# Performance work log

Hardware: AMD Instinct MI355X
Metric: run time of the kernel (lower is better)

Reference implementation:

```python
import jax, jax.numpy as jnp
import numpy as np

V, D, H, O = 32000, 256, 512, 6
B, T = 128, 2048


def setup_inputs() -> dict:
    key = jax.random.key(0)
    ks = jax.random.split(key, 8)
    s = lambda k, shp, fan: jax.random.normal(k, shp, jnp.float32) / np.float32(np.sqrt(fan))
    return dict(
        token_ids=jax.random.randint(ks[0], (B, T), 0, V),
        emb=s(ks[1], (V, D), D),
        gru_wih=s(ks[2], (3 * H, D), D),
        gru_whh=s(ks[3], (3 * H, H), H),
        gru_b=jnp.zeros((3 * H,), jnp.float32),
        gru_bn=jnp.zeros((H,), jnp.float32),
        lstm_wih=s(ks[4], (4 * H, H), H),
        lstm_whh=s(ks[5], (4 * H, H), H),
        lstm_b=jnp.zeros((4 * H,), jnp.float32),
        head_w=s(ks[6], (O, H), H),
        head_b=jnp.zeros((O,), jnp.float32),
    )


def reference(token_ids, emb, gru_wih, gru_whh, gru_b, gru_bn,
              lstm_wih, lstm_whh, lstm_b, head_w, head_b):
    x = emb[token_ids]                      # (B, T, D) embedding lookup
    xs = jnp.swapaxes(x, 0, 1)              # (T, B, D) for scan over time
    h = gru_whh.shape[1]
    h0 = jnp.zeros((x.shape[0], h), x.dtype)

    def step(carry, xt):
        hg, hl, cl = carry
        # --- equinox GRUCell ---
        ig = xt @ gru_wih.T + gru_b         # (B, 3H)
        hh = hg @ gru_whh.T                 # (B, 3H)
        ir, iz, inn = jnp.split(ig, 3, axis=-1)
        hr, hz, hn = jnp.split(hh, 3, axis=-1)
        r = jax.nn.sigmoid(ir + hr)
        z = jax.nn.sigmoid(iz + hz)
        n = jnp.tanh(inn + r * (hn + gru_bn))
        hg_new = n + z * (hg - n)           # == (1-z)*n + z*hg
        # --- equinox LSTMCell (input = GRU output) ---
        lin = hg_new @ lstm_wih.T + hl @ lstm_whh.T + lstm_b  # (B, 4H)
        i_, f_, g_, o_ = jnp.split(lin, 4, axis=-1)
        c_new = jax.nn.sigmoid(f_) * cl + jax.nn.sigmoid(i_) * jnp.tanh(g_)
        h_new = jax.nn.sigmoid(o_) * jnp.tanh(c_new)
        return (hg_new, h_new, c_new), None

    (_, h_final, _), _ = jax.lax.scan(step, (h0, h0, h0), xs)
    return h_final @ head_w.T + head_b      # (B, O)
```

## Files before the change

### kernel.cpp

```cpp
#include <hip/hip_runtime.h>
#include <hip/hip_bf16.h>


typedef short v8s __attribute__((ext_vector_type(8)));
typedef float v4f __attribute__((ext_vector_type(4)));
typedef unsigned long long u64;

#define T_STEPS 2048
#define RING_OFF 8192
#define DYN_LDS 150816

#define MFMA16(a, b, c) __builtin_amdgcn_mfma_f32_16x16x32_bf16((a), (b), (c), 0, 0, 0)

__device__ __forceinline__ v4f v4zero() { v4f z = {0.f, 0.f, 0.f, 0.f}; return z; }
__device__ __forceinline__ float sigf(float x) { return 1.f / (1.f + __expf(-x)); }
__device__ __forceinline__ float tanhf_fast(float x) { return 1.f - 2.f / (1.f + __expf(2.f * x)); }

__device__ __forceinline__ ushort f2us(float v) {
  __hip_bfloat16 b = __float2bfloat16(v);
  return *reinterpret_cast<ushort*>(&b);
}
__device__ __forceinline__ float us2f(ushort u) {
  __hip_bfloat16 b;
  *reinterpret_cast<ushort*>(&b) = u;
  return __bfloat162float(b);
}
__device__ __forceinline__ void cvt_hilo(float v, ushort& h, ushort& l) {
  __hip_bfloat16 bh = __float2bfloat16(v);
  float r = v - __bfloat162float(bh);
  __hip_bfloat16 bl = __float2bfloat16(r);
  h = *reinterpret_cast<ushort*>(&bh);
  l = *reinterpret_cast<ushort*>(&bl);
}
__device__ __forceinline__ void stage4(ushort* hi, ushort* lo, const float* src) {
  float4 v = *(const float4*)src;
  float a[4] = {v.x, v.y, v.z, v.w};
#pragma unroll
  for (int j = 0; j < 4; ++j) { ushort h, l; cvt_hilo(a[j], h, l); hi[j] = h; lo[j] = l; }
}
__device__ __forceinline__ void stage4h(ushort* hi, const float* src) {
  float4 v = *(const float4*)src;
  float a[4] = {v.x, v.y, v.z, v.w};
#pragma unroll
  for (int j = 0; j < 4; ++j) hi[j] = f2us(a[j]);
}
__device__ __forceinline__ void st_wt(ushort* p, ushort v) {
  __hip_atomic_store(p, v, __ATOMIC_RELAXED, __HIP_MEMORY_SCOPE_AGENT);
}
__device__ __forceinline__ void st_row32(ushort* rowp, int r16, ushort uh) {
  unsigned v32 = (unsigned)uh;
  unsigned nb = (unsigned)__shfl_xor((int)v32, 1);
  if (!(r16 & 1)) v32 |= (nb << 16);
  unsigned hi32 = (unsigned)__shfl_xor((int)v32, 2);
  if ((r16 & 3) == 0) {
    u64 v = (u64)v32 | ((u64)hi32 << 32);
    __hip_atomic_store((u64*)(rowp + r16), v, __ATOMIC_RELAXED, __HIP_MEMORY_SCOPE_AGENT);
  }
}
__device__ __forceinline__ v8s ld_a16(const ushort* p) {
  u64 a = __hip_atomic_load((const u64*)p, __ATOMIC_RELAXED, __HIP_MEMORY_SCOPE_AGENT);
  u64 b = __hip_atomic_load((const u64*)p + 1, __ATOMIC_RELAXED, __HIP_MEMORY_SCOPE_AGENT);
  union { u64 u[2]; v8s v; } r;
  r.u[0] = a; r.u[1] = b;
  return r.v;
}

__device__ __forceinline__ int poll_ge(const int* p, int tgt, long& budget) {
  while (budget > 0) {
    if (__hip_atomic_load(p, __ATOMIC_RELAXED, __HIP_MEMORY_SCOPE_AGENT) >= tgt) return 1;
    __builtin_amdgcn_s_sleep(1);
    --budget;
  }
  return 0;
}
__device__ __forceinline__ int pollep(const int* gepo, int ta,
                                      const int* lepo, int tb,
                                      int lane, long& budget, int& slack) {
  const int* p = (lane < 32) ? (gepo + lane) : (lepo + (lane - 32));
  const int t = (lane < 32) ? ta : tb;
  while (budget > 0) {
    int v = __hip_atomic_load(p, __ATOMIC_RELAXED, __HIP_MEMORY_SCOPE_AGENT);
    int d = v - t;
    if (__all(d >= 0)) {
      int m = d;
#pragma unroll
      for (int off = 1; off < 64; off <<= 1) {
        int o = __shfl_xor(m, off);
        m = (o < m) ? o : m;
      }
      slack = m;
      return 1;
    }
    __builtin_amdgcn_s_sleep(1);
    --budget;
  }
  return 0;
}

__global__ void __launch_bounds__(256, 1) rnn_persistent(
    const int* __restrict__ tok,
    const float* __restrict__ emb,
    const float* __restrict__ gwih,
    const float* __restrict__ gwhh,
    const float* __restrict__ gb,
    const float* __restrict__ gbn,
    const float* __restrict__ lwih,
    const float* __restrict__ lwhh,
    const float* __restrict__ lb,
    char* __restrict__ ws,
    int hstride, int has_lo)
{
  extern __shared__ char smem[];
  const int tid  = threadIdx.x;
  const int wgid = blockIdx.x;
  const bool is_gru = (wgid < 64);
  const int sub = is_gru ? wgid : (wgid - 64);
  const int bg  = sub & 1;
  const int cg  = sub >> 1;
  const int colbase = cg * 16;
  const int b0 = bg * 64;
  const int lane = tid & 63;
  const int wave = tid >> 6;
  const int quad = lane >> 4;
  const int r16  = lane & 15;

  int* cnt = (int*)ws;
  int* gru_ep  = cnt + bg * 32;
  int* lstm_ep = cnt + 64 + bg * 32;
  int* boot    = cnt + 128;
  ushort* ring = (ushort*)(ws + RING_OFF);
  const int slotE = 128 * hstride;
  ushort* hlb = ring + 2 * slotE;

  const int mrow  = wave * 16 + r16;
  const int bglob = b0 + wave * 16 + quad * 4;
  const int col   = colbase + r16;
  long budget = 3000000;
  int slack = 0;

  if (is_gru) {
    ushort* smemU = (ushort*)smem;
    const int WIH_HI = 0, WIH_LO = 12672, WHH_HI = 25344, WHH_LO = 50304;
    int* okf = (int*)(smem + 150528);

    for (int i = tid; i < 48 * 64; i += 256) {
      int row = i >> 6, q = (i & 63) * 4;
      int gate = row >> 4, c = colbase + (row & 15);
      stage4(&smemU[WIH_HI + row * 264 + q], &smemU[WIH_LO + row * 264 + q],
             gwih + (long)(gate * 512 + c) * 256 + q);
    }
    for (int i = tid; i < 48 * 128; i += 256) {
      int row = i >> 7, k = (i & 127) * 4;
      int gate = row >> 4, c = colbase + (row & 15);
      stage4(&smemU[WHH_HI + row * 520 + k], &smemU[WHH_LO + row * 520 + k],
             gwhh + (long)(gate * 512 + c) * 512 + k);
    }
    const float b_r  = gb[col];
    const float b_z  = gb[512 + col];
    const float b_in = gb[1024 + col];
    const float bnv  = gbn[col];
    __syncthreads();

    if (tid == 0) {
      __hip_atomic_fetch_add(boot, 1, __ATOMIC_RELEASE, __HIP_MEMORY_SCOPE_AGENT);
      long bb = 3000000;
      okf[0] = poll_ge(boot, 128, bb);
    }
    __syncthreads();
    if (!okf[0]) { if (wgid == 0 && tid == 0) st_wt(&hlb[slotE + 0], f2us(1.0e4f)); return; }

    v4f acc_r, acc_z, acc_nx;
    float hgreg[4] = {0.f, 0.f, 0.f, 0.f};
    float4 xa[16];

    auto prefetch_x = [&](int tn) {
      int ntok = tok[(b0 + mrow) * T_STEPS + tn];
      const float* xrow = emb + (long)ntok * 256;
#pragma unroll
      for (int kk = 0; kk < 8; ++kk) {
        xa[2 * kk]     = *(const float4*)(xrow + kk * 32 + quad * 8);
        xa[2 * kk + 1] = *(const float4*)(xrow + kk * 32 + quad * 8 + 4);
      }
    };
    auto accx_compute = [&]() {
      acc_r = v4zero(); acc_z = v4zero(); acc_nx = v4zero();
#pragma unroll
      for (int kk = 0; kk < 8; ++kk) {
        float xv[8] = {xa[2 * kk].x, xa[2 * kk].y, xa[2 * kk].z, xa[2 * kk].w,
                       xa[2 * kk + 1].x, xa[2 * kk + 1].y, xa[2 * kk + 1].z, xa[2 * kk + 1].w};
        v8s ahi, alo;
#pragma unroll
        for (int j = 0; j < 8; ++j) { ushort h, l; cvt_hilo(xv[j], h, l); ahi[j] = (short)h; alo[j] = (short)l; }
        const int orr = (r16) * 264 + kk * 32 + quad * 8;
        const int oz  = (16 + r16) * 264 + kk * 32 + quad * 8;
        const int on  = (32 + r16) * 264 + kk * 32 + quad * 8;
        v8s brh = *(const v8s*)&smemU[WIH_HI + orr], brl = *(const v8s*)&smemU[WIH_LO + orr];
        v8s bzh = *(const v8s*)&smemU[WIH_HI + oz],  bzl = *(const v8s*)&smemU[WIH_LO + oz];
        v8s bnh = *(const v8s*)&smemU[WIH_HI + on],  bnl = *(const v8s*)&smemU[WIH_LO + on];
        acc_r = MFMA16(ahi, brh, acc_r); acc_r = MFMA16(alo, brh, acc_r); acc_r = MFMA16(ahi, brl, acc_r);
        acc_z = MFMA16(ahi, bzh, acc_z); acc_z = MFMA16(alo, bzh, acc_z); acc_z = MFMA16(ahi, bzl, acc_z);
        acc_nx = MFMA16(ahi, bnh, acc_nx); acc_nx = MFMA16(alo, bnh, acc_nx); acc_nx = MFMA16(ahi, bnl, acc_nx);
      }
    };

    prefetch_x(0);
    accx_compute();

    for (int t = 0; t < T_STEPS; ++t) {
      if (t + 1 < T_STEPS) prefetch_x(t + 1);

      if (t > 0) {
        if (wave == 0) {
          int ok = 1;
          if (slack > 0) { --slack; }
          else ok = pollep(gru_ep, t, lstm_ep, t - 1, lane, budget, slack);
          if (lane == 0) okf[0] = ok;
        }
        __syncthreads();
        if (!okf[0]) { if (tid == 0) st_wt(&hlb[slotE + 2 + wgid], f2us(100.f)); break; }
      }

      v8s ahi[16], alo[16];
      if (t > 0) {
        const ushort* hrow = ring + ((t - 1) & 1) * slotE + (b0 + mrow) * hstride;
#pragma unroll
        for (int kk = 0; kk < 16; ++kk) {
          ahi[kk] = ld_a16(&hrow[kk * 32 + quad * 8]);
          if (has_lo) alo[kk] = ld_a16(&hrow[512 + kk * 32 + quad * 8]);
        }
      }

      v4f acc_nh = v4zero();
      if (t > 0) {
#pragma unroll
        for (int kk = 0; kk < 16; ++kk) {
          const int orr = (r16) * 520 + kk * 32 + quad * 8;
          const int oz  = (16 + r16) * 520 + kk * 32 + quad * 8;
          const int on  = (32 + r16) * 520 + kk * 32 + quad * 8;
          v8s brh = *(const v8s*)&smemU[WHH_HI + orr], brl = *(const v8s*)&smemU[WHH_LO + orr];
          v8s bzh = *(const v8s*)&smemU[WHH_HI + oz],  bzl = *(const v8s*)&smemU[WHH_LO + oz];
          v8s bnh = *(const v8s*)&smemU[WHH_HI + on],  bnl = *(const v8s*)&smemU[WHH_LO + on];
          acc_r = MFMA16(ahi[kk], brh, acc_r); acc_r = MFMA16(ahi[kk], brl, acc_r);
          acc_z = MFMA16(ahi[kk], bzh, acc_z); acc_z = MFMA16(ahi[kk], bzl, acc_z);
          acc_nh = MFMA16(ahi[kk], bnh, acc_nh); acc_nh = MFMA16(ahi[kk], bnl, acc_nh);
          if (has_lo) {
            acc_r = MFMA16(alo[kk], brh, acc_r);
            acc_z = MFMA16(alo[kk], bzh, acc_z);
            acc_nh = MFMA16(alo[kk], bnh, acc_nh);
          }
        }
      }

      ushort* slotT = ring + (t & 1) * slotE;
#pragma unroll
      for (int rg = 0; rg < 4; ++rg) {
        float r = sigf(acc_r[rg] + b_r);
        float z = sigf(acc_z[rg] + b_z);
        float nn = tanhf_fast(acc_nx[rg] + b_in + r * (acc_nh[rg] + bnv));
        float hnew = nn + z * (hgreg[rg] - nn);
        hgreg[rg] = hnew;
        ushort uh = f2us(hnew);
        ushort* rp = &slotT[(bglob + rg) * hstride + colbase];
        st_row32(rp, r16, uh);
        if (has_lo) st_row32(rp + 512, r16, f2us(hnew - us2f(uh)));
      }

      __syncthreads();
      if (tid == 0)
        __hip_atomic_store(gru_ep + cg, t + 1, __ATOMIC_RELEASE, __HIP_MEMORY_SCOPE_AGENT);
      if (t + 1 < T_STEPS) accx_compute();
    }
  } else {
    ushort* smemU = (ushort*)smem;
    int* okf = (int*)(smem + 132096);

    for (int i = tid; i < 64 * 256; i += 256) {
      int row = i >> 8, k = (i & 255) * 4;
      int gate = row >> 4, c = colbase + (row & 15);
      long grow = gate * 512 + c;
      const float* src = (k < 512) ? (lwih + grow * 512 + k) : (lwhh + grow * 512 + (k - 512));
      stage4h(&smemU[row * 1032 + k], src);
    }
    const float b_i = lb[col];
    const float b_f = lb[512 + col];
    const float b_g = lb[1024 + col];
    const float b_o = lb[1536 + col];
    __syncthreads();

    if (tid == 0) {
      __hip_atomic_fetch_add(boot, 1, __ATOMIC_RELEASE, __HIP_MEMORY_SCOPE_AGENT);
      long bb = 3000000;
      okf[0] = poll_ge(boot, 128, bb);
    }
    __syncthreads();
    if (!okf[0]) { if (wgid == 64 && tid == 0) st_wt(&hlb[slotE + 1], f2us(1.0e4f)); return; }

    float creg[4] = {0.f, 0.f, 0.f, 0.f};

    for (int t = 0; t < T_STEPS; ++t) {
      if (wave == 0) {
        int ok = 1;
        if (slack > 0) { --slack; }
        else ok = pollep(gru_ep, t + 1, lstm_ep, t, lane, budget, slack);
        if (lane == 0) okf[0] = ok;
      }
      __syncthreads();
      if (!okf[0]) { if (tid == 0) st_wt(&hlb[slotE + 2 + wgid], f2us(100.f)); break; }

      v8s ghi[16], glo[16];
      {
        const ushort* hrow = ring + (t & 1) * slotE + (b0 + mrow) * hstride;
#pragma unroll
        for (int kk = 0; kk < 16; ++kk) {
          ghi[kk] = ld_a16(&hrow[kk * 32 + quad * 8]);
          if (has_lo) glo[kk] = ld_a16(&hrow[512 + kk * 32 + quad * 8]);
        }
      }
      v8s lhi[16], llo[16];
      const ushort* lrow = hlb + ((t - 1) & 1) * slotE + (b0 + mrow) * hstride;
      if (t > 0) {
#pragma unroll
        for (int kk = 0; kk < 16; ++kk) lhi[kk] = ld_a16(&lrow[kk * 32 + quad * 8]);
      }

      v4f ai = v4zero(), af = v4zero(), ag = v4zero(), ao = v4zero();
#pragma unroll
      for (int kk = 0; kk < 16; ++kk) {
        v8s bi = *(const v8s*)&smemU[(r16) * 1032 + kk * 32 + quad * 8];
        v8s bf = *(const v8s*)&smemU[(16 + r16) * 1032 + kk * 32 + quad * 8];
        v8s bgv = *(const v8s*)&smemU[(32 + r16) * 1032 + kk * 32 + quad * 8];
        v8s bo = *(const v8s*)&smemU[(48 + r16) * 1032 + kk * 32 + quad * 8];
        ai = MFMA16(ghi[kk], bi, ai); af = MFMA16(ghi[kk], bf, af);
        ag = MFMA16(ghi[kk], bgv, ag); ao = MFMA16(ghi[kk], bo, ao);
        if (has_lo) {
          ai = MFMA16(glo[kk], bi, ai); af = MFMA16(glo[kk], bf, af);
          ag = MFMA16(glo[kk], bgv, ag); ao = MFMA16(glo[kk], bo, ao);
        }
      }

      if (t > 0) {
        if (has_lo) {
#pragma unroll
          for (int kk = 0; kk < 16; ++kk) llo[kk] = ld_a16(&lrow[512 + kk * 32 + quad * 8]);
        }
#pragma unroll
        for (int kk = 0; kk < 16; ++kk) {
          v8s bi = *(const v8s*)&smemU[(r16) * 1032 + 512 + kk * 32 + quad * 8];
          v8s bf = *(const v8s*)&smemU[(16 + r16) * 1032 + 512 + kk * 32 + quad * 8];
          v8s bgv = *(const v8s*)&smemU[(32 + r16) * 1032 + 512 + kk * 32 + quad * 8];
          v8s bo = *(const v8s*)&smemU[(48 + r16) * 1032 + 512 + kk * 32 + quad * 8];
          ai = MFMA16(lhi[kk], bi, ai); af = MFMA16(lhi[kk], bf, af);
          ag = MFMA16(lhi[kk], bgv, ag); ao = MFMA16(lhi[kk], bo, ao);
        }
        if (has_lo) {
#pragma unroll
          for (int kk = 0; kk < 16; ++kk) {
            v8s bi = *(const v8s*)&smemU[(r16) * 1032 + 512 + kk * 32 + quad * 8];
            v8s bf = *(const v8s*)&smemU[(16 + r16) * 1032 + 512 + kk * 32 + quad * 8];
            v8s bgv = *(const v8s*)&smemU[(32 + r16) * 1032 + 512 + kk * 32 + quad * 8];
            v8s bo = *(const v8s*)&smemU[(48 + r16) * 1032 + 512 + kk * 32 + quad * 8];
            ai = MFMA16(llo[kk], bi, ai); af = MFMA16(llo[kk], bf, af);
            ag = MFMA16(llo[kk], bgv, ag); ao = MFMA16(llo[kk], bo, ao);
          }
        }
      }

      ushort* hout = hlb + (t & 1) * slotE;
#pragma unroll
      for (int rg = 0; rg < 4; ++rg) {
        float i_ = sigf(ai[rg] + b_i), f_ = sigf(af[rg] + b_f);
        float g_ = tanhf_fast(ag[rg] + b_g), o_ = sigf(ao[rg] + b_o);
        float cn = f_ * creg[rg] + i_ * g_;
        creg[rg] = cn;
        float hv = o_ * tanhf_fast(cn);
        ushort uh = f2us(hv);
        ushort* rp = &hout[(bglob + rg) * hstride + colbase];
        st_row32(rp, r16, uh);
        if (has_lo) st_row32(rp + 512, r16, f2us(hv - us2f(uh)));
      }

      __syncthreads();
      if (tid == 0)
        __hip_atomic_store(lstm_ep + cg, t + 1, __ATOMIC_RELEASE, __HIP_MEMORY_SCOPE_AGENT);
    }
  }
}

__global__ void head_kernel(const char* __restrict__ ws,
                            const float* __restrict__ hw,
                            const float* __restrict__ hbias,
                            float* __restrict__ out,
                            int hstride, int has_lo) {
  const ushort* h1 = (const ushort*)(ws + RING_OFF) + 3 * 128 * hstride;
  const int b = blockIdx.x, l = threadIdx.x;
  const int k0 = l * 8;
  v8s hi = ld_a16(&h1[b * hstride + k0]);
  v8s lo;
  if (has_lo) lo = ld_a16(&h1[b * hstride + 512 + k0]);
  float acc[6] = {0.f, 0.f, 0.f, 0.f, 0.f, 0.f};
#pragma unroll
  for (int j = 0; j < 8; ++j) {
    float h = us2f((ushort)hi[j]);
    if (has_lo) h += us2f((ushort)lo[j]);
#pragma unroll
    for (int o = 0; o < 6; ++o) acc[o] += h * hw[o * 512 + k0 + j];
  }
#pragma unroll
  for (int o = 0; o < 6; ++o) {
    float v = acc[o];
    for (int off = 32; off > 0; off >>= 1) v += __shfl_down(v, off);
    if (l == 0) out[b * 6 + o] = v + hbias[o];
  }
}

__global__ void init_ws(int* cnt) {
  int i = blockIdx.x * blockDim.x + threadIdx.x;
  if (i < 2048)
    __hip_atomic_store(cnt + i, 0, __ATOMIC_RELAXED, __HIP_MEMORY_SCOPE_AGENT);
}

__global__ void ws_too_small_marker(float* out) {
  if (threadIdx.x == 0 && blockIdx.x == 0) out[0] = 12345.0f;
}

extern "C" void kernel_launch(void* const* d_in, const int* in_sizes, int n_in,
                              void* d_out, int out_size, void* d_ws, size_t ws_size,
                              hipStream_t stream) {
  const int*   tok  = (const int*)d_in[0];
  const float* emb  = (const float*)d_in[1];
  const float* gwih = (const float*)d_in[2];
  const float* gwhh = (const float*)d_in[3];
  const float* gb   = (const float*)d_in[4];
  const float* gbn  = (const float*)d_in[5];
  const float* lwih = (const float*)d_in[6];
  const float* lwhh = (const float*)d_in[7];
  const float* lb   = (const float*)d_in[8];
  const float* hw   = (const float*)d_in[9];
  const float* hb   = (const float*)d_in[10];

  (void)in_sizes; (void)n_in; (void)out_size;

  const size_t WS_A = (size_t)RING_OFF + 4ull * 128 * 1024 * 2;
  const size_t WS_B = (size_t)RING_OFF + 4ull * 128 * 512 * 2;
  if (ws_size < WS_B) {
    hipLaunchKernelGGL(ws_too_small_marker, dim3(1), dim3(64), 0, stream, (float*)d_out);
    return;
  }
  const int has_lo  = (ws_size >= (size_t)WS_A) ? 1 : 0;
  const int hstride = has_lo ? 1024 : 512;

  (void)hipFuncSetAttribute(reinterpret_cast<const void*>(rnn_persistent),
                            hipFuncAttributeMaxDynamicSharedMemorySize, DYN_LDS);
  hipLaunchKernelGGL(init_ws, dim3(8), dim3(256), 0, stream, (int*)d_ws);
  hipLaunchKernelGGL(rnn_persistent, dim3(128), dim3(256), DYN_LDS, stream,
                     tok, emb, gwih, gwhh, gb, gbn, lwih, lwhh, lb,
                     (char*)d_ws, hstride, has_lo);
  hipLaunchKernelGGL(head_kernel, dim3(128), dim3(64), 0, stream,
                     (const char*)d_ws, hw, hb, (float*)d_out, hstride, has_lo);
}
```

Baseline: 37.06 ms.

## Replace workgroup barriers with per-wave epoch flags for cross-block step sync

Measured after the change: 50.38 ms. 35.9% more time.

```diff
diff --git a/kernel.cpp b/kernel.cpp
--- a/kernel.cpp
+++ b/kernel.cpp
@@ -73,10 +73,10 @@
   }
   return 0;
 }
-__device__ __forceinline__ int pollep(const int* gepo, int ta,
-                                      const int* lepo, int tb,
+__device__ __forceinline__ int pollep(const int* gline, int ta,
+                                      const int* lline, int tb,
                                       int lane, long& budget, int& slack) {
-  const int* p = (lane < 32) ? (gepo + lane) : (lepo + (lane - 32));
+  const int* p = (lane < 32) ? (gline + lane) : (lline + (lane - 32));
   const int t = (lane < 32) ? ta : tb;
   while (budget > 0) {
     int v = __hip_atomic_load(p, __ATOMIC_RELAXED, __HIP_MEMORY_SCOPE_AGENT);
@@ -91,7 +91,7 @@
       slack = m;
       return 1;
     }
-    __builtin_amdgcn_s_sleep(1);
+    __builtin_amdgcn_s_sleep(2);
     --budget;
   }
   return 0;
@@ -125,9 +125,9 @@
   const int r16  = lane & 15;
 
   int* cnt = (int*)ws;
-  int* gru_ep  = cnt + bg * 32;
-  int* lstm_ep = cnt + 64 + bg * 32;
-  int* boot    = cnt + 128;
+  int* gline = cnt + (bg * 4 + wave) * 32;
+  int* lline = cnt + 256 + (bg * 4 + wave) * 32;
+  int* boot  = cnt + 512;
   ushort* ring = (ushort*)(ws + RING_OFF);
   const int slotE = 128 * hstride;
   ushort* hlb = ring + 2 * slotE;
@@ -210,14 +210,11 @@
       if (t + 1 < T_STEPS) prefetch_x(t + 1);
 
       if (t > 0) {
-        if (wave == 0) {
-          int ok = 1;
-          if (slack > 0) { --slack; }
-          else ok = pollep(gru_ep, t, lstm_ep, t - 1, lane, budget, slack);
-          if (lane == 0) okf[0] = ok;
-        }
-        __syncthreads();
-        if (!okf[0]) { if (tid == 0) st_wt(&hlb[slotE + 2 + wgid], f2us(100.f)); break; }
+        if (slack > 0) { --slack; }
+        else if (!pollep(gline, t, lline, t - 1, lane, budget, slack)) {
+          if (lane == 0) st_wt(&hlb[slotE + 2 + wgid], f2us(100.f));
+          break;
+        }
       }
 
       v8s ahi[16], alo[16];
@@ -265,9 +262,8 @@
         if (has_lo) st_row32(rp + 512, r16, f2us(hnew - us2f(uh)));
       }
 
-      __syncthreads();
-      if (tid == 0)
-        __hip_atomic_store(gru_ep + cg, t + 1, __ATOMIC_RELEASE, __HIP_MEMORY_SCOPE_AGENT);
+      if (lane == 0)
+        __hip_atomic_store(gline + cg, t + 1, __ATOMIC_RELEASE, __HIP_MEMORY_SCOPE_AGENT);
       if (t + 1 < T_STEPS) accx_compute();
     }
   } else {
@@ -298,14 +294,11 @@
     float creg[4] = {0.f, 0.f, 0.f, 0.f};
 
     for (int t = 0; t < T_STEPS; ++t) {
-      if (wave == 0) {
-        int ok = 1;
-        if (slack > 0) { --slack; }
-        else ok = pollep(gru_ep, t + 1, lstm_ep, t, lane, budget, slack);
-        if (lane == 0) okf[0] = ok;
-      }
-      __syncthreads();
-      if (!okf[0]) { if (tid == 0) st_wt(&hlb[slotE + 2 + wgid], f2us(100.f)); break; }
+      if (slack > 0) { --slack; }
+      else if (!pollep(gline, t + 1, lline, t, lane, budget, slack)) {
+        if (lane == 0) st_wt(&hlb[slotE + 2 + wgid], f2us(100.f));
+        break;
+      }
 
       v8s ghi[16], glo[16];
       {
@@ -379,9 +372,8 @@
         if (has_lo) st_row32(rp + 512, r16, f2us(hv - us2f(uh)));
       }
 
-      __syncthreads();
-      if (tid == 0)
-        __hip_atomic_store(lstm_ep + cg, t + 1, __ATOMIC_RELEASE, __HIP_MEMORY_SCOPE_AGENT);
+      if (lane == 0)
+        __hip_atomic_store(lline + cg, t + 1, __ATOMIC_RELEASE, __HIP_MEMORY_SCOPE_AGENT);
     }
   }
 }
```
